# Performance work log

Measured on AMD Instinct MI355X. Metric: run time of the kernel, lower is better.

## Reference

```python
import jax, jax.numpy as jnp
import numpy as np

EMBED_DIM = 1024
NUM_HEADS = 16
D_K = EMBED_DIM // NUM_HEADS
FFN_DIM = 4096
EPS = 1e-5


def _linear_params(key, fan_in, fan_out):
    kw, kb = jax.random.split(key)
    bound = 1.0 / np.sqrt(fan_in)
    W = jax.random.uniform(kw, (fan_out, fan_in), jnp.float32, -bound, bound)
    b = jax.random.uniform(kb, (fan_out,), jnp.float32, -bound, bound)
    return W, b


def setup_inputs() -> dict:
    key = jax.random.key(0)
    ks = jax.random.split(key, 8)
    x = jax.random.normal(ks[0], (2, 2048, EMBED_DIM), jnp.float32)
    Wq, bq = _linear_params(ks[1], EMBED_DIM, EMBED_DIM)
    Wk, bk = _linear_params(ks[2], EMBED_DIM, EMBED_DIM)
    Wv, bv = _linear_params(ks[3], EMBED_DIM, EMBED_DIM)
    Wo, bo = _linear_params(ks[4], EMBED_DIM, EMBED_DIM)
    W1, b1 = _linear_params(ks[5], EMBED_DIM, FFN_DIM)
    W2, b2 = _linear_params(ks[6], FFN_DIM, EMBED_DIM)
    g1 = jnp.ones((EMBED_DIM,), jnp.float32)
    be1 = jnp.zeros((EMBED_DIM,), jnp.float32)
    g2 = jnp.ones((EMBED_DIM,), jnp.float32)
    be2 = jnp.zeros((EMBED_DIM,), jnp.float32)
    return {"x": x, "Wq": Wq, "bq": bq, "Wk": Wk, "bk": bk, "Wv": Wv, "bv": bv,
            "Wo": Wo, "bo": bo, "W1": W1, "b1": b1, "W2": W2, "b2": b2,
            "g1": g1, "be1": be1, "g2": g2, "be2": be2}


def _layernorm(x, g, b):
    mu = jnp.mean(x, axis=-1, keepdims=True)
    var = jnp.var(x, axis=-1, keepdims=True)
    return (x - mu) * jax.lax.rsqrt(var + EPS) * g + b


def reference(x, Wq, bq, Wk, bk, Wv, bv, Wo, bo, W1, b1, W2, b2, g1, be1, g2, be2):
    B, S, _ = x.shape
    h = _layernorm(x, g1, be1)
    # qkv projections -> [B, H, S, d_k]
    def split_heads(t):
        return t.reshape(B, S, NUM_HEADS, D_K).transpose(0, 2, 1, 3)
    q = split_heads(h @ Wq.T + bq)
    k = split_heads(h @ Wk.T + bk)
    v = split_heads(h @ Wv.T + bv)
    scores = jnp.einsum('bhqd,bhkd->bhqk', q, k) / np.sqrt(D_K).astype(np.float32)
    attn = jax.nn.softmax(scores, axis=-1)
    out = jnp.einsum('bhqk,bhkd->bhqd', attn, v)
    out = out.transpose(0, 2, 1, 3).reshape(B, S, EMBED_DIM)
    attn_out = out @ Wo.T + bo
    x = x + attn_out
    h2 = _layernorm(x, g2, be2)
    ffn = jax.nn.relu(h2 @ W1.T + b1) @ W2.T + b2
    return x + ffn
```

## Files before the change

kernel.cpp:

```cpp
#include <hip/hip_runtime.h>

typedef __attribute__((ext_vector_type(8))) short short8;
typedef __attribute__((ext_vector_type(4))) float f32x4;
typedef __attribute__((ext_vector_type(4))) unsigned short us4;

#define MFMA_BF16(a, b, c) __builtin_amdgcn_mfma_f32_16x16x32_bf16((a), (b), (c), 0, 0, 0)

__device__ __forceinline__ unsigned short f2bf(float f) {
  union { float f; unsigned int u; } x; x.f = f;
  unsigned int r = x.u + 0x7FFFu + ((x.u >> 16) & 1u);
  return (unsigned short)(r >> 16);
}
__device__ __forceinline__ float bf2f(unsigned short b) {
  union { float f; unsigned int u; } x; x.u = ((unsigned int)b) << 16;
  return x.f;
}

typedef __attribute__((address_space(3))) unsigned int lds_uint;
typedef const __attribute__((address_space(1))) unsigned int gbl_uint;

__device__ __forceinline__ void gload_lds16(const void* g, void* l) {
  __builtin_amdgcn_global_load_lds((gbl_uint*)g, (lds_uint*)l, 16, 0, 0);
}

__device__ __forceinline__ short8 lds_swz_read(const unsigned short* base, int row, int colbyte) {
  return *(const short8*)((const char*)base + row * 128 + (colbyte ^ ((row & 7) << 4)));
}

__global__ __launch_bounds__(256) void cvt_ln(const float* __restrict__ Wq,
                                              const float* __restrict__ Wk,
                                              const float* __restrict__ Wv,
                                              const float* __restrict__ Wo,
                                              const float* __restrict__ W1,
                                              const float* __restrict__ W2,
                                              unsigned short* __restrict__ Wqkv_b,
                                              unsigned short* __restrict__ Wo_b,
                                              unsigned short* __restrict__ W1_b,
                                              unsigned short* __restrict__ W2_b,
                                              const float* __restrict__ x,
                                              const float* __restrict__ g,
                                              const float* __restrict__ be,
                                              unsigned short* __restrict__ lnout) {
  const int b = blockIdx.x;
  const int t = threadIdx.x;
  __shared__ float red[8];
  if (b < 12288) {
    const float* src;
    unsigned short* dst;
    int off;
    if (b < 1024)      { src = Wq; dst = Wqkv_b;           off = b; }
    else if (b < 2048) { src = Wk; dst = Wqkv_b + 1048576; off = b - 1024; }
    else if (b < 3072) { src = Wv; dst = Wqkv_b + 2097152; off = b - 2048; }
    else if (b < 4096) { src = Wo; dst = Wo_b;             off = b - 3072; }
    else if (b < 8192) { src = W1; dst = W1_b;             off = b - 4096; }
    else               { src = W2; dst = W2_b;             off = b - 8192; }
    const int i = off * 256 + t;
    const float4 v = ((const float4*)src)[i];
    us4 o;
    o.x = f2bf(v.x); o.y = f2bf(v.y); o.z = f2bf(v.z); o.w = f2bf(v.w);
    ((us4*)dst)[i] = o;
    return;
  }
  const int row = b - 12288;
  const float4 v = ((const float4*)(x + (size_t)row * 1024))[t];
  float s = v.x + v.y + v.z + v.w;
  float s2 = v.x * v.x + v.y * v.y + v.z * v.z + v.w * v.w;
#pragma unroll
  for (int d = 1; d < 64; d <<= 1) {
    s += __shfl_xor(s, d);
    s2 += __shfl_xor(s2, d);
  }
  const int wid = t >> 6, lane = t & 63;
  if (lane == 0) { red[wid] = s; red[4 + wid] = s2; }
  __syncthreads();
  s = red[0] + red[1] + red[2] + red[3];
  s2 = red[4] + red[5] + red[6] + red[7];
  const float mu = s * (1.0f / 1024.0f);
  const float var = s2 * (1.0f / 1024.0f) - mu * mu;
  const float rstd = rsqrtf(var + 1e-5f);
  const float4 gv = ((const float4*)g)[t];
  const float4 bv = ((const float4*)be)[t];
  us4 o;
  o.x = f2bf((v.x - mu) * rstd * gv.x + bv.x);
  o.y = f2bf((v.y - mu) * rstd * gv.y + bv.y);
  o.z = f2bf((v.z - mu) * rstd * gv.z + bv.z);
  o.w = f2bf((v.w - mu) * rstd * gv.w + bv.w);
  ((us4*)(lnout + (size_t)row * 1024))[t] = o;
}

__global__ __launch_bounds__(256) void ln_kernel(const float* __restrict__ x,
                                                 const float* __restrict__ g,
                                                 const float* __restrict__ be,
                                                 unsigned short* __restrict__ out) {
  const int row = blockIdx.x;
  const int t = threadIdx.x;
  const float4 v = ((const float4*)(x + (size_t)row * 1024))[t];
  float s = v.x + v.y + v.z + v.w;
  float s2 = v.x * v.x + v.y * v.y + v.z * v.z + v.w * v.w;
#pragma unroll
  for (int d = 1; d < 64; d <<= 1) {
    s += __shfl_xor(s, d);
    s2 += __shfl_xor(s2, d);
  }
  __shared__ float red[8];
  const int wid = t >> 6, lane = t & 63;
  if (lane == 0) { red[wid] = s; red[4 + wid] = s2; }
  __syncthreads();
  s = red[0] + red[1] + red[2] + red[3];
  s2 = red[4] + red[5] + red[6] + red[7];
  const float mu = s * (1.0f / 1024.0f);
  const float var = s2 * (1.0f / 1024.0f) - mu * mu;
  const float rstd = rsqrtf(var + 1e-5f);
  const float4 gv = ((const float4*)g)[t];
  const float4 bv = ((const float4*)be)[t];
  us4 o;
  o.x = f2bf((v.x - mu) * rstd * gv.x + bv.x);
  o.y = f2bf((v.y - mu) * rstd * gv.y + bv.y);
  o.z = f2bf((v.z - mu) * rstd * gv.z + bv.z);
  o.w = f2bf((v.w - mu) * rstd * gv.w + bv.w);
  ((us4*)(out + (size_t)row * 1024))[t] = o;
}

__global__ __launch_bounds__(256) void ffn2_reduce(float* __restrict__ out,
                                                   const unsigned short* __restrict__ p0,
                                                   const unsigned short* __restrict__ p1,
                                                   const float* __restrict__ x1,
                                                   const float* __restrict__ b2) {
  const int row = blockIdx.x, t = threadIdx.x;
  const size_t i = (size_t)row * 256 + t;
  const us4 a0 = ((const us4*)p0)[i];
  const us4 a1 = ((const us4*)p1)[i];
  const float4 c = ((const float4*)x1)[i];
  const float4 b = ((const float4*)b2)[t];
  float4 v;
  v.x = bf2f(a0.x) + bf2f(a1.x) + c.x + b.x;
  v.y = bf2f(a0.y) + bf2f(a1.y) + c.y + b.y;
  v.z = bf2f(a0.z) + bf2f(a1.z) + c.z + b.z;
  v.w = bf2f(a0.w) + bf2f(a1.w) + c.w + b.w;
  ((float4*)out)[i] = v;
}

template <int BN, int EPI, int MINW = 2>
__global__ __launch_bounds__(256, MINW) void gemm_bf16(const unsigned short* __restrict__ A,
                                                       const unsigned short* __restrict__ B,
                                                       const float* __restrict__ bias,
                                                       const float* __restrict__ biasK,
                                                       const float* __restrict__ biasV,
                                                       const float* __restrict__ res,
                                                       void* __restrict__ outp,
                                                       int M, int N, int K,
                                                       int gx, int gy, int kspl) {
  constexpr int WN = (BN == 128) ? 2 : 1;
  constexpr int WROWS = 128 / (4 / WN);
  constexpr int MW = WROWS / 16;
  constexpr int NW = (BN / WN) / 16;
  constexpr int BCH = BN / 32;
  constexpr int LOADS = 4 + BCH;

  __shared__ __align__(16) unsigned short SMEM[2 * 128 * 64 + 2 * BN * 64];
  auto As = (unsigned short(*)[128 * 64])SMEM;
  auto Bs = (unsigned short(*)[BN * 64])(SMEM + 2 * 128 * 64);

  const int nwg = gridDim.x;
  const int id2 = ((int)blockIdx.x & 7) * (nwg >> 3) + ((int)blockIdx.x >> 3);
  const int bx = id2 % gx;
  const int byz = id2 / gx;
  const int by = byz % gy;
  const int bz = byz / gy;

  const int wid = threadIdx.x >> 6;
  const int lane = threadIdx.x & 63;
  const int lr = lane & 15, lg = lane >> 4;
  const int row0 = by * 128;
  const int col0 = bx * BN;
  const int k0 = bz * kspl;
  const int wm = (wid / WN) * WROWS;
  const int wn = (wid % WN) * (BN / WN);

  const int scol = ((lane & 7) ^ ((lane >> 3) & 7)) * 8;

  auto stage = [&](int buf, int kt) {
#pragma unroll
    for (int i = 0; i < 4; ++i) {
      const int r = wid * 32 + i * 8;
      gload_lds16(A + (size_t)(row0 + r + (lane >> 3)) * K + kt + scol,
                  (void*)&As[buf][r * 64]);
    }
#pragma unroll
    for (int i = 0; i < BCH; ++i) {
      const int r = wid * (8 * BCH) + i * 8;
      gload_lds16(B + (size_t)(col0 + r + (lane >> 3)) * K + kt + scol,
                  (void*)&Bs[buf][r * 64]);
    }
  };

  f32x4 acc[MW][NW];
#pragma unroll
  for (int m = 0; m < MW; ++m)
#pragma unroll
    for (int n = 0; n < NW; ++n) acc[m][n] = (f32x4){0.f, 0.f, 0.f, 0.f};

  auto mma = [&](int buf) {
#pragma unroll
    for (int kk = 0; kk < 64; kk += 32) {
      const int colbyte = kk * 2 + lg * 16;
      short8 av[MW], bv[NW];
#pragma unroll
      for (int m = 0; m < MW; ++m)
        av[m] = lds_swz_read(&As[buf][0], wm + m * 16 + lr, colbyte);
#pragma unroll
      for (int n = 0; n < NW; ++n)
        bv[n] = lds_swz_read(&Bs[buf][0], wn + n * 16 + lr, colbyte);
#pragma unroll
      for (int m = 0; m < MW; ++m)
#pragma unroll
        for (int n = 0; n < NW; ++n) acc[m][n] = MFMA_BF16(av[m], bv[n], acc[m][n]);
    }
  };

  stage(0, k0);
  stage(1, k0 + 64);
  const int ktend = k0 + kspl;
  int cur = 0;
  for (int kt = k0; kt < ktend - 64; kt += 64) {
    asm volatile("s_waitcnt vmcnt(%0)" ::"i"(LOADS) : "memory");
    __builtin_amdgcn_s_barrier();
    __builtin_amdgcn_sched_barrier(0);
    mma(cur);
    __builtin_amdgcn_s_barrier();
    if (kt + 128 < ktend) stage(cur, kt + 128);
    cur ^= 1;
  }
  asm volatile("s_waitcnt vmcnt(0)" ::: "memory");
  __builtin_amdgcn_s_barrier();
  __builtin_amdgcn_sched_barrier(0);
  mma(cur);

  if constexpr (EPI == 0) {
    const int which = col0 >> 10;
    if (which < 2) {
#pragma unroll
      for (int m = 0; m < MW; ++m)
#pragma unroll
        for (int n = 0; n < NW; ++n)
#pragma unroll
          for (int r = 0; r < 4; ++r) {
            const int row = row0 + wm + m * 16 + lg * 4 + r;
            const int col = col0 + wn + n * 16 + lr;
            const int c = col & 1023;
            const float* bp = (which == 0) ? bias : biasK;
            const float v = acc[m][n][r] + bp[c];
            const size_t idx = (size_t)which * 4194304 +
                ((((size_t)(row >> 11)) * 16 + (c >> 6)) * 2048 + (row & 2047)) * 64 +
                (c & 63);
            ((unsigned short*)outp)[idx] = f2bf(v);
          }
    } else {
      unsigned short* Vlds = SMEM;
      __syncthreads();
#pragma unroll
      for (int m = 0; m < MW; ++m)
#pragma unroll
        for (int n = 0; n < NW; ++n)
#pragma unroll
          for (int r = 0; r < 4; ++r) {
            const int rl = wm + m * 16 + lg * 4 + r;
            const int xx = rl & 63;
            const int rs = (rl & ~63) | ((xx & 15) << 2) | (xx >> 4);
            const int coll = wn + n * 16 + lr;
            const float v = acc[m][n][r] + biasV[(col0 & 1023) + coll];
            Vlds[coll * 144 + rs] = f2bf(v);
          }
      __syncthreads();
      const int cl = threadIdx.x >> 1, h = threadIdx.x & 1;
      const int c = (col0 & 1023) + cl;
      const int bb = row0 >> 11;
      unsigned short* vdst = (unsigned short*)outp + (size_t)2 * 4194304 +
          (((size_t)bb * 16 + (c >> 6)) * 64 + (c & 63)) * 2048 + (row0 & 2047) + h * 64;
#pragma unroll
      for (int w = 0; w < 8; ++w)
        *(short8*)(vdst + w * 8) = *(const short8*)&Vlds[cl * 144 + h * 64 + w * 8];
    }
  } else {
#pragma unroll
    for (int m = 0; m < MW; ++m) {
#pragma unroll
      for (int n = 0; n < NW; ++n) {
#pragma unroll
        for (int r = 0; r < 4; ++r) {
          const int row = row0 + wm + m * 16 + lg * 4 + r;
          const int col = col0 + wn + n * 16 + lr;
          if constexpr (EPI == 1) {
            const float v = acc[m][n][r] + bias[col];
            ((unsigned short*)outp)[(size_t)row * N + col] = f2bf(fmaxf(v, 0.f));
          } else {
            const float v = acc[m][n][r] + bias[col];
            ((float*)outp)[(size_t)row * N + col] = v + res[(size_t)row * N + col];
          }
        }
      }
    }
  }
}

template <int BM, int BN, int EPI>
__global__ __launch_bounds__(512, 2) void gemm256(const unsigned short* __restrict__ A,
                                                  const unsigned short* __restrict__ B,
                                                  const float* __restrict__ bias,
                                                  void* __restrict__ part,
                                                  void* __restrict__ outp,
                                                  int M, int N, int K,
                                                  int gx, int gy, int kspl) {
  constexpr int MW = BM / 32;
  constexpr int NW = BN / 64;
  constexpr int A_ISS = BM / 64;
  constexpr int B_ISS = BN / 64;
  constexpr int LOADS = A_ISS + B_ISS;

  __shared__ __align__(16) unsigned short As[2][BM * 64];
  __shared__ __align__(16) unsigned short Bs[2][BN * 64];

  const int nwg = gridDim.x;
  const int id2 = ((int)blockIdx.x & 7) * (nwg >> 3) + ((int)blockIdx.x >> 3);
  const int bx = id2 % gx;
  const int byz = id2 / gx;
  const int by = byz % gy;
  const int bz = byz / gy;

  const int wid = threadIdx.x >> 6;
  const int lane = threadIdx.x & 63;
  const int lr = lane & 15, lg = lane >> 4;
  const int wr = wid >> 2, wc = wid & 3;
  const int row0 = by * BM;
  const int col0 = bx * BN;
  const int k0 = bz * kspl;
  const int wm = wr * (BM / 2);
  const int wn = wc * (BN / 4);

  const int scol = ((lane & 7) ^ ((lane >> 3) & 7)) * 8;

  auto stage = [&](int buf, int kt) {
#pragma unroll
    for (int i = 0; i < A_ISS; ++i) {
      const int r = wid * 8 + i * 64;
      gload_lds16(A + (size_t)(row0 + r + (lane >> 3)) * K + kt + scol,
                  (void*)&As[buf][r * 64]);
    }
#pragma unroll
    for (int i = 0; i < B_ISS; ++i) {
      const int r = wid * 8 + i * 64;
      gload_lds16(B + (size_t)(col0 + r + (lane >> 3)) * K + kt + scol,
                  (void*)&Bs[buf][r * 64]);
    }
  };

  f32x4 acc[MW][NW];
#pragma unroll
  for (int m = 0; m < MW; ++m)
#pragma unroll
    for (int n = 0; n < NW; ++n) acc[m][n] = (f32x4){0.f, 0.f, 0.f, 0.f};

  auto mma = [&](int buf) {
#pragma unroll
    for (int kk = 0; kk < 64; kk += 32) {
      const int colbyte = kk * 2 + lg * 16;
      short8 av[MW], bv[NW];
#pragma unroll
      for (int m = 0; m < MW; ++m)
        av[m] = lds_swz_read(&As[buf][0], wm + m * 16 + lr, colbyte);
#pragma unroll
      for (int n = 0; n < NW; ++n)
        bv[n] = lds_swz_read(&Bs[buf][0], wn + n * 16 + lr, colbyte);
#pragma unroll
      for (int m = 0; m < MW; ++m)
#pragma unroll
        for (int n = 0; n < NW; ++n) acc[m][n] = MFMA_BF16(av[m], bv[n], acc[m][n]);
    }
  };

  stage(0, k0);
  stage(1, k0 + 64);
  const int ktend = k0 + kspl;
  int cur = 0;
  for (int kt = k0; kt < ktend - 64; kt += 64) {
    asm volatile("s_waitcnt vmcnt(%0)" ::"i"(LOADS) : "memory");
    __builtin_amdgcn_s_barrier();
    __builtin_amdgcn_sched_barrier(0);
    mma(cur);
    __builtin_amdgcn_s_barrier();
    if (kt + 128 < ktend) stage(cur, kt + 128);
    cur ^= 1;
  }
  asm volatile("s_waitcnt vmcnt(0)" ::: "memory");
  __builtin_amdgcn_s_barrier();
  __builtin_amdgcn_sched_barrier(0);
  mma(cur);

#pragma unroll
  for (int m = 0; m < MW; ++m) {
#pragma unroll
    for (int n = 0; n < NW; ++n) {
#pragma unroll
      for (int r = 0; r < 4; ++r) {
        const int row = row0 + wm + m * 16 + lg * 4 + r;
        const int col = col0 + wn + n * 16 + lr;
        if constexpr (EPI == 1) {
          const float v = acc[m][n][r] + bias[col];
          ((unsigned short*)outp)[(size_t)row * N + col] = f2bf(fmaxf(v, 0.f));
        } else {
          unsigned short* dst = (unsigned short*)(bz ? part : outp);
          dst[(size_t)row * N + col] = f2bf(acc[m][n][r]);
        }
      }
    }
  }
}

__global__ __launch_bounds__(256, 2) void attn_kernel(const unsigned short* __restrict__ q,
                                                      const unsigned short* __restrict__ k,
                                                      const unsigned short* __restrict__ vt,
                                                      unsigned short* __restrict__ o) {
  const int bh = blockIdx.x;
  const int q0 = blockIdx.y * 128;
  const unsigned short* qh = q + (size_t)bh * 2048 * 64;
  const unsigned short* kh = k + (size_t)bh * 2048 * 64;
  const unsigned short* vh = vt + (size_t)bh * 64 * 2048;
  const int wid = threadIdx.x >> 6, lane = threadIdx.x & 63;
  const int lr = lane & 15, lg = lane >> 4;
  const int qw = q0 + wid * 32;

  __shared__ __align__(16) unsigned short Vt[2][64 * 64];
  __shared__ __align__(16) unsigned short Ps[4][32 * 64];

  constexpr float CS = 0.125f * 1.4426950408889634f;
  short8 qf[2][2];
#pragma unroll
  for (int m = 0; m < 2; ++m)
#pragma unroll
    for (int kk = 0; kk < 2; ++kk) {
      short8 t = *(const short8*)&qh[(size_t)(qw + m * 16 + lr) * 64 + kk * 32 + lg * 8];
#pragma unroll
      for (int j = 0; j < 8; ++j) t[j] = (short)f2bf(bf2f((unsigned short)t[j]) * CS);
      qf[m][kk] = t;
    }

  f32x4 po[2][4];
  float lrun[2][4];
#pragma unroll
  for (int m = 0; m < 2; ++m) {
#pragma unroll
    for (int n = 0; n < 4; ++n) po[m][n] = (f32x4){0.f, 0.f, 0.f, 0.f};
#pragma unroll
    for (int r = 0; r < 4; ++r) lrun[m][r] = 0.f;
  }

  const int scol = ((lane & 7) ^ ((lane >> 3) & 7)) * 8;
  char* const PsB = (char*)&Ps[wid][0];

  short8 kfA[4][2], kfB[4][2];

#define LOAD_K(KF, kt)                                                                   \
  {                                                                                      \
    _Pragma("unroll") for (int n = 0; n < 4; ++n) _Pragma("unroll") for (int kk = 0;     \
                                                                         kk < 2; ++kk)  \
        KF[n][kk] =                                                                      \
        *(const short8*)&kh[(size_t)((kt) + n * 16 + lr) * 64 + kk * 32 + lg * 8];       \
  }
#define STAGE_VT(BUF, kt)                                                                \
  {                                                                                      \
    _Pragma("unroll") for (int i = 0; i < 2; ++i) {                                      \
      const int r = (wid * 2 + i) * 8;                                                   \
      gload_lds16(vh + (size_t)(r + (lane >> 3)) * 2048 + (kt) + scol,                   \
                  (void*)&Vt[BUF][r * 64]);                                              \
    }                                                                                    \
  }

  LOAD_K(kfA, 0)
  STAGE_VT(0, 0)

#define STEP(KC, KN, BUF, t)                                                             \
  {                                                                                      \
    f32x4 sc[2][4];                                                                      \
    _Pragma("unroll") for (int m = 0; m < 2; ++m) _Pragma("unroll") for (int n = 0;      \
                                                                         n < 4; ++n)    \
        sc[m][n] = (f32x4){0.f, 0.f, 0.f, 0.f};                                          \
    __builtin_amdgcn_s_setprio(1);                                                       \
    _Pragma("unroll") for (int kk = 0; kk < 2; ++kk)                                     \
        _Pragma("unroll") for (int m = 0; m < 2; ++m)                                    \
        _Pragma("unroll") for (int n = 0; n < 4; ++n)                                    \
        sc[m][n] = MFMA_BF16(qf[m][kk], KC[n][kk], sc[m][n]);                            \
    __builtin_amdgcn_s_setprio(0);                                                       \
    const int ktn = ((t) + 1 < 32) ? ((t) + 1) * 64 : 0;                                 \
    LOAD_K(KN, ktn)                                                                      \
    _Pragma("unroll") for (int m = 0; m < 2; ++m)                                        \
        _Pragma("unroll") for (int r = 0; r < 4; ++r) {                                  \
      const float p0 = __builtin_amdgcn_exp2f(sc[m][0][r]);                              \
      const float p1 = __builtin_amdgcn_exp2f(sc[m][1][r]);                              \
      const float p2 = __builtin_amdgcn_exp2f(sc[m][2][r]);                              \
      const float p3 = __builtin_amdgcn_exp2f(sc[m][3][r]);                              \
      lrun[m][r] += (p0 + p1) + (p2 + p3);                                               \
      unsigned int u0, u1;                                                               \
      asm("v_cvt_pk_bf16_f32 %0, %1, %2" : "=v"(u0) : "v"(p0), "v"(p1));                 \
      asm("v_cvt_pk_bf16_f32 %0, %1, %2" : "=v"(u1) : "v"(p2), "v"(p3));                 \
      const int row = m * 16 + lg * 4 + r;                                               \
      uint2 pk2; pk2.x = u0; pk2.y = u1;                                                 \
      *(uint2*)(PsB + row * 128 + ((lr * 8) ^ ((row & 7) << 4))) = pk2;                  \
    }                                                                                    \
    asm volatile("s_waitcnt vmcnt(8) lgkmcnt(0)" ::: "memory");                          \
    __builtin_amdgcn_s_barrier();                                                        \
    __builtin_amdgcn_sched_barrier(0);                                                   \
    STAGE_VT(BUF ^ 1, ktn)                                                               \
    __builtin_amdgcn_sched_barrier(0);                                                   \
    _Pragma("unroll") for (int kk = 0; kk < 2; ++kk) {                                   \
      const int coff = kk * 64 + lg * 16;                                                \
      short8 pa[2], vbr[4];                                                              \
      _Pragma("unroll") for (int m = 0; m < 2; ++m) {                                    \
        const int prow = m * 16 + lr;                                                    \
        pa[m] = *(const short8*)(PsB + prow * 128 + (coff ^ ((prow & 7) << 4)));         \
      }                                                                                  \
      _Pragma("unroll") for (int n = 0; n < 4; ++n)                                      \
        vbr[n] = lds_swz_read(&Vt[BUF][0], n * 16 + lr, coff);                           \
      __builtin_amdgcn_s_setprio(1);                                                     \
      _Pragma("unroll") for (int m = 0; m < 2; ++m)                                      \
          _Pragma("unroll") for (int n = 0; n < 4; ++n)                                  \
          po[m][n] = MFMA_BF16(pa[m], vbr[n], po[m][n]);                                 \
      __builtin_amdgcn_s_setprio(0);                                                     \
    }                                                                                    \
  }

  for (int t = 0; t < 32; t += 2) {
    STEP(kfA, kfB, 0, t)
    STEP(kfB, kfA, 1, t + 1)
  }
#undef STEP
#undef LOAD_K
#undef STAGE_VT

#pragma unroll
  for (int d = 1; d < 16; d <<= 1)
#pragma unroll
    for (int m = 0; m < 2; ++m)
#pragma unroll
      for (int r = 0; r < 4; ++r) lrun[m][r] += __shfl_xor(lrun[m][r], d);

  const int b = bh >> 4, hh = bh & 15;
#pragma unroll
  for (int m = 0; m < 2; ++m)
#pragma unroll
    for (int n = 0; n < 4; ++n)
#pragma unroll
      for (int r = 0; r < 4; ++r) {
        const int qrow = qw + m * 16 + lg * 4 + r;
        const int d = n * 16 + lr;
        o[((size_t)b * 2048 + qrow) * 1024 + hh * 64 + d] =
            f2bf(po[m][n][r] / lrun[m][r]);
      }
}

extern "C" void kernel_launch(void* const* d_in, const int* in_sizes, int n_in,
                              void* d_out, int out_size, void* d_ws, size_t ws_size,
                              hipStream_t stream) {
  const float* x  = (const float*)d_in[0];
  const float* Wq = (const float*)d_in[1];
  const float* bq = (const float*)d_in[2];
  const float* Wk = (const float*)d_in[3];
  const float* bk = (const float*)d_in[4];
  const float* Wv = (const float*)d_in[5];
  const float* bv = (const float*)d_in[6];
  const float* Wo = (const float*)d_in[7];
  const float* bo = (const float*)d_in[8];
  const float* W1 = (const float*)d_in[9];
  const float* b1 = (const float*)d_in[10];
  const float* W2 = (const float*)d_in[11];
  const float* b2 = (const float*)d_in[12];
  const float* g1 = (const float*)d_in[13];
  const float* be1 = (const float*)d_in[14];
  const float* g2 = (const float*)d_in[15];
  const float* be2 = (const float*)d_in[16];

  char* ws = (char*)d_ws;
  const size_t MB = 1024 * 1024;
  unsigned short* Wqkv_b = (unsigned short*)(ws + 0 * MB);
  unsigned short* Wo_b   = (unsigned short*)(ws + 6 * MB);
  unsigned short* W1_b   = (unsigned short*)(ws + 8 * MB);
  unsigned short* W2_b   = (unsigned short*)(ws + 16 * MB);
  unsigned short* h_b    = (unsigned short*)(ws + 24 * MB);
  unsigned short* qb     = (unsigned short*)(ws + 32 * MB);
  unsigned short* ab     = (unsigned short*)(ws + 56 * MB);
  float*          x1     = (float*)(ws + 64 * MB);
  unsigned short* fb     = (unsigned short*)(ws + 32 * MB);
  unsigned short* p0     = (unsigned short*)(ws + 0 * MB);
  unsigned short* p1     = (unsigned short*)(ws + 8 * MB);

  cvt_ln<<<16384, 256, 0, stream>>>(Wq, Wk, Wv, Wo, W1, W2, Wqkv_b, Wo_b, W1_b, W2_b,
                                    x, g1, be1, h_b);

  gemm_bf16<128, 0><<<768, 256, 0, stream>>>(h_b, Wqkv_b, bq, bk, bv, nullptr, qb,
                                             4096, 3072, 1024, 24, 32, 1024);

  attn_kernel<<<dim3(32, 16), 256, 0, stream>>>(qb, qb + 4194304, qb + 2 * 4194304, ab);

  gemm_bf16<64, 2, 3><<<512, 256, 0, stream>>>(ab, Wo_b, bo, nullptr, nullptr, x, x1,
                                               4096, 1024, 1024, 16, 32, 1024);

  ln_kernel<<<4096, 256, 0, stream>>>(x1, g2, be2, h_b);

  gemm256<256, 256, 1><<<256, 512, 0, stream>>>(h_b, W1_b, b1, nullptr, fb,
                                                4096, 4096, 1024, 16, 16, 1024);

  gemm256<128, 256, 4><<<256, 512, 0, stream>>>(fb, W2_b, nullptr, p1, p0,
                                                4096, 1024, 4096, 4, 32, 2048);

  ffn2_reduce<<<4096, 256, 0, stream>>>((float*)d_out, p0, p1, x1, b2);
}
```

Measured before the change: 234.7 us.

## Software-pipeline attention loop: compute QK^T for next tile before exp of current

Restructures the attention inner loop so the QK^T MFMAs for tile t+1 are issued before the exp/softmax work of tile t, with double-buffered score registers and K fragments loaded two tiles ahead. The goal is to overlap the transcendental and LDS-store work with matrix-core work and to hide K load latency. It raises register pressure (two score buffers and two K fragment sets live at once), which may lower occupancy. It also adds a peeled prologue and epilogue.

```diff
diff --git a/kernel.cpp b/kernel.cpp
--- a/kernel.cpp
+++ b/kernel.cpp
@@ -458,6 +458,7 @@
   char* const PsB = (char*)&Ps[wid][0];
 
   short8 kfA[4][2], kfB[4][2];
+  f32x4 scA[2][4], scB[2][4];
 
 #define LOAD_K(KF, kt)                                                                   \
   {                                                                                      \
@@ -474,30 +475,26 @@
                   (void*)&Vt[BUF][r * 64]);                                              \
     }                                                                                    \
   }
-
-  LOAD_K(kfA, 0)
-  STAGE_VT(0, 0)
-
-#define STEP(KC, KN, BUF, t)                                                             \
+#define QKT(SC, KF)                                                                      \
   {                                                                                      \
-    f32x4 sc[2][4];                                                                      \
     _Pragma("unroll") for (int m = 0; m < 2; ++m) _Pragma("unroll") for (int n = 0;      \
                                                                          n < 4; ++n)    \
-        sc[m][n] = (f32x4){0.f, 0.f, 0.f, 0.f};                                          \
+        SC[m][n] = (f32x4){0.f, 0.f, 0.f, 0.f};                                          \
     __builtin_amdgcn_s_setprio(1);                                                       \
     _Pragma("unroll") for (int kk = 0; kk < 2; ++kk)                                     \
         _Pragma("unroll") for (int m = 0; m < 2; ++m)                                    \
         _Pragma("unroll") for (int n = 0; n < 4; ++n)                                    \
-        sc[m][n] = MFMA_BF16(qf[m][kk], KC[n][kk], sc[m][n]);                            \
+        SC[m][n] = MFMA_BF16(qf[m][kk], KF[n][kk], SC[m][n]);                            \
     __builtin_amdgcn_s_setprio(0);                                                       \
-    const int ktn = ((t) + 1 < 32) ? ((t) + 1) * 64 : 0;                                 \
-    LOAD_K(KN, ktn)                                                                      \
+  }
+#define EXPP(SC)                                                                         \
+  {                                                                                      \
     _Pragma("unroll") for (int m = 0; m < 2; ++m)                                        \
         _Pragma("unroll") for (int r = 0; r < 4; ++r) {                                  \
-      const float p0 = __builtin_amdgcn_exp2f(sc[m][0][r]);                              \
-      const float p1 = __builtin_amdgcn_exp2f(sc[m][1][r]);                              \
-      const float p2 = __builtin_amdgcn_exp2f(sc[m][2][r]);                              \
-      const float p3 = __builtin_amdgcn_exp2f(sc[m][3][r]);                              \
+      const float p0 = __builtin_amdgcn_exp2f(SC[m][0][r]);                              \
+      const float p1 = __builtin_amdgcn_exp2f(SC[m][1][r]);                              \
+      const float p2 = __builtin_amdgcn_exp2f(SC[m][2][r]);                              \
+      const float p3 = __builtin_amdgcn_exp2f(SC[m][3][r]);                              \
       lrun[m][r] += (p0 + p1) + (p2 + p3);                                               \
       unsigned int u0, u1;                                                               \
       asm("v_cvt_pk_bf16_f32 %0, %1, %2" : "=v"(u0) : "v"(p0), "v"(p1));                 \
@@ -506,11 +503,9 @@
       uint2 pk2; pk2.x = u0; pk2.y = u1;                                                 \
       *(uint2*)(PsB + row * 128 + ((lr * 8) ^ ((row & 7) << 4))) = pk2;                  \
     }                                                                                    \
-    asm volatile("s_waitcnt vmcnt(8) lgkmcnt(0)" ::: "memory");                          \
-    __builtin_amdgcn_s_barrier();                                                        \
-    __builtin_amdgcn_sched_barrier(0);                                                   \
-    STAGE_VT(BUF ^ 1, ktn)                                                               \
-    __builtin_amdgcn_sched_barrier(0);                                                   \
+  }
+#define PV(BUF)                                                                          \
+  {                                                                                      \
     _Pragma("unroll") for (int kk = 0; kk < 2; ++kk) {                                   \
       const int coff = kk * 64 + lg * 16;                                                \
       short8 pa[2], vbr[4];                                                              \
@@ -528,11 +523,40 @@
     }                                                                                    \
   }
 
-  for (int t = 0; t < 32; t += 2) {
-    STEP(kfA, kfB, 0, t)
-    STEP(kfB, kfA, 1, t + 1)
-  }
+  LOAD_K(kfA, 0)
+  STAGE_VT(0, 0)
+  LOAD_K(kfB, 64)
+  QKT(scA, kfA)
+
+#define STEP(KN, KL, SCe, SCf, BUF, t)                                                   \
+  {                                                                                      \
+    QKT(SCf, KN)                                                                         \
+    const int kt2 = ((t) + 2 < 32) ? ((t) + 2) * 64 : 0;                                 \
+    LOAD_K(KL, kt2)                                                                      \
+    EXPP(SCe)                                                                            \
+    asm volatile("s_waitcnt vmcnt(8) lgkmcnt(0)" ::: "memory");                          \
+    __builtin_amdgcn_s_barrier();                                                        \
+    __builtin_amdgcn_sched_barrier(0);                                                   \
+    const int ktn = ((t) + 1 < 32) ? ((t) + 1) * 64 : 0;                                 \
+    STAGE_VT(BUF ^ 1, ktn)                                                               \
+    __builtin_amdgcn_sched_barrier(0);                                                   \
+    PV(BUF)                                                                              \
+  }
+
+  for (int t = 0; t < 30; t += 2) {
+    STEP(kfB, kfA, scA, scB, 0, t)
+    STEP(kfA, kfB, scB, scA, 1, t + 1)
+  }
+  STEP(kfB, kfA, scA, scB, 0, 30)
+  EXPP(scB)
+  asm volatile("s_waitcnt vmcnt(0) lgkmcnt(0)" ::: "memory");
+  __builtin_amdgcn_s_barrier();
+  __builtin_amdgcn_sched_barrier(0);
+  PV(1)
 #undef STEP
+#undef PV
+#undef EXPP
+#undef QKT
 #undef LOAD_K
 #undef STAGE_VT
 
```

New measurement: 231.7 us. About the same (-1.3%).
